# Kernel optimization log

Measured on AMD Instinct MI355X. Metric: run time of the kernel, lower is better.

The kernel has to match this reference:

```python
import jax, jax.numpy as jnp
import numpy as np

NUM_EMBEDDINGS = 1024
EMBEDDING_DIM = 64
COMMITMENT_COST = 0.25


def setup_inputs() -> dict:
    key = jax.random.key(0)
    k1, k2 = jax.random.split(key)
    inputs = jax.random.normal(k1, (16, 64, 64, 64), dtype=jnp.float32)
    codebook = jax.random.normal(k2, (EMBEDDING_DIM, NUM_EMBEDDINGS), dtype=jnp.float32) * 0.01
    return {"inputs": inputs, "codebook": codebook}


def reference(inputs, codebook):
    # flatten exactly as torch: reshape(-1, D) on (B,C,H,W)
    flat = inputs.reshape(-1, EMBEDDING_DIM)  # [N, D]
    distances = (jnp.sum(flat * flat, axis=1, keepdims=True)
                 + jnp.sum(codebook * codebook, axis=0, keepdims=True)
                 - 2.0 * jnp.matmul(flat, codebook))
    encoding_indices = jnp.argmin(distances, axis=1)  # [N]
    quantized = codebook[:, encoding_indices].T.reshape(inputs.shape)
    # losses (MSE over all elements)
    codebook_loss = jnp.mean((jax.lax.stop_gradient(quantized) - inputs) ** 2)
    commitment_loss = COMMITMENT_COST * jnp.mean((quantized - jax.lax.stop_gradient(inputs)) ** 2)
    # perplexity from codebook usage histogram
    n = encoding_indices.shape[0]
    counts = jnp.zeros((NUM_EMBEDDINGS,), dtype=jnp.float32).at[encoding_indices].add(1.0)
    avg_probs = counts / n
    entropy = -jnp.sum(avg_probs * jnp.log(avg_probs + 1e-10))
    perplexity = jnp.exp(entropy)
    # straight-through estimator
    ste = inputs + jax.lax.stop_gradient(quantized - inputs)
    return (ste, perplexity, codebook_loss, commitment_loss,
            encoding_indices.reshape(inputs.shape[0], -1))
```

## Files before the change

kernel.cpp:

```cpp
#include <hip/hip_runtime.h>

typedef __attribute__((ext_vector_type(8))) short short8;
typedef __attribute__((ext_vector_type(4))) float f32x4;

#define N_ROWS   65536
#define DIM      64
#define K_CODES  1024
#define TOTAL_ELEMS 4194304
#define THETA    1e-3f
#define ROWS_PB  64


__device__ __forceinline__ unsigned short f2bf(float f) {
    union { float f; unsigned int u; } c; c.f = f;
    unsigned int u = c.u;
    return (unsigned short)((u + 0x7fffu + ((u >> 16) & 1u)) >> 16);
}
__device__ __forceinline__ float bf2f(unsigned short b) {
    union { unsigned int u; float f; } c; c.u = ((unsigned int)b) << 16;
    return c.f;
}
__device__ __forceinline__ f32x4 MFMA(short8 a, short8 b, f32x4 c) {
    return __builtin_amdgcn_mfma_f32_16x16x32_bf16(a, b, c, 0, 0, 0);
}

__global__ __launch_bounds__(64) void k_prep(const float* __restrict__ cb,
                                             float* __restrict__ norms,
                                             int* __restrict__ counts,
                                             float* __restrict__ cbT,
                                             unsigned short* __restrict__ cb_hi,
                                             unsigned short* __restrict__ cb_lo,
                                             int* __restrict__ flagcnt) {
    int k = blockIdx.x * 64 + threadIdx.x;
    float v[64];
#pragma unroll
    for (int d = 0; d < DIM; ++d) v[d] = cb[d * K_CODES + k];
    float s = __fmul_rn(v[0], v[0]);
#pragma unroll
    for (int d = 1; d < DIM; ++d) s = __fadd_rn(s, __fmul_rn(v[d], v[d]));
    norms[k] = s;
#pragma unroll
    for (int d = 0; d < DIM; ++d) {
        cbT[k * DIM + d] = v[d];
        float t = -2.0f * v[d];
        unsigned short hb = f2bf(t);
        cb_hi[k * DIM + d] = hb;
        cb_lo[k * DIM + d] = f2bf(t - bf2f(hb));
    }
    counts[k] = 0;
    if (k == 0) flagcnt[0] = 0;
}

__global__ __launch_bounds__(256, 2) void k_assign(const float* __restrict__ x,
                                                   const float* __restrict__ norms,
                                                   const unsigned short* __restrict__ cb_hi,
                                                   const unsigned short* __restrict__ cb_lo,
                                                   int* __restrict__ idx_out,
                                                   int* __restrict__ flagcnt,
                                                   int* __restrict__ flaglist) {
    __shared__ __align__(16) unsigned short xs_hi[64 * 64];
    __shared__ __align__(16) unsigned short xs_lo[64 * 64];
    __shared__ float xxs[64];
    __shared__ float mv1[4][64];
    __shared__ float mv2[4][64];
    __shared__ int   mk1[4][64];

    const int tid = threadIdx.x;
    const int r0 = blockIdx.x * 64;
    const int wave = tid >> 6, lane = tid & 63;
    const int lr = lane & 15, lg = lane >> 4;

#pragma unroll
    for (int i = 0; i < 2; ++i) {
        int c = i * 256 + tid;
        int row = c >> 3, ch = c & 7;
        const float4* src = reinterpret_cast<const float4*>(x + (size_t)(r0 + row) * DIM + ch * 8);
        float4 f0 = src[0], f1 = src[1];
        float f[8] = {f0.x, f0.y, f0.z, f0.w, f1.x, f1.y, f1.z, f1.w};
        union { short8 v; unsigned short u[8]; } h, l;
#pragma unroll
        for (int j = 0; j < 8; ++j) {
            unsigned short hb = f2bf(f[j]);
            h.u[j] = hb;
            l.u[j] = f2bf(f[j] - bf2f(hb));
        }
        int eo = row * 64 + ((((ch * 16) ^ ((row & 7) << 4))) >> 1);
        *reinterpret_cast<short8*>(&xs_hi[eo]) = h.v;
        *reinterpret_cast<short8*>(&xs_lo[eo]) = l.v;
    }
    if (lane < 16) {
        int row = wave * 16 + lane;
        const float* xr = x + (size_t)(r0 + row) * DIM;
        float r[8];
#pragma unroll
        for (int j = 0; j < 8; ++j) { float v = xr[j]; r[j] = __fmul_rn(v, v); }
#pragma unroll
        for (int m = 1; m < 8; ++m)
#pragma unroll
            for (int j = 0; j < 8; ++j) { float v = xr[8 * m + j]; r[j] = __fadd_rn(r[j], __fmul_rn(v, v)); }
        float t01 = __fadd_rn(r[0], r[1]), t23 = __fadd_rn(r[2], r[3]);
        float t45 = __fadd_rn(r[4], r[5]), t67 = __fadd_rn(r[6], r[7]);
        xxs[row] = __fadd_rn(__fadd_rn(t01, t23), __fadd_rn(t45, t67));
    }
    __syncthreads();

    short8 a_hi[4][2], a_lo[4][2];
#pragma unroll
    for (int rt = 0; rt < 4; ++rt)
#pragma unroll
        for (int kh = 0; kh < 2; ++kh) {
            int row = rt * 16 + lr;
            int bo = (kh * 64 + lg * 16) ^ ((row & 7) << 4);
            int eo = row * 64 + (bo >> 1);
            a_hi[rt][kh] = *reinterpret_cast<const short8*>(&xs_hi[eo]);
            a_lo[rt][kh] = *reinterpret_cast<const short8*>(&xs_lo[eo]);
        }
    float xxv[16];
#pragma unroll
    for (int rt = 0; rt < 4; ++rt)
#pragma unroll
        for (int r = 0; r < 4; ++r) xxv[rt * 4 + r] = xxs[rt * 16 + lg * 4 + r];

    float v1[16], v2[16]; int k1[16];
#pragma unroll
    for (int i = 0; i < 16; ++i) { v1[i] = 3.4e38f; v2[i] = 3.4e38f; k1[i] = 0; }

    const short8* ph = reinterpret_cast<const short8*>(cb_hi) + (size_t)(wave * 256 + lr) * 8;
    const short8* pl = reinterpret_cast<const short8*>(cb_lo) + (size_t)(wave * 256 + lr) * 8;
    const float*  pe = norms + wave * 256 + lr;

    short8 nh0 = ph[lg], nh1 = ph[4 + lg];
    short8 nl0 = pl[lg], nl1 = pl[4 + lg];
    float  nee = *pe;

    for (int ct = 0; ct < 16; ++ct) {
        short8 h0 = nh0, h1 = nh1, l0 = nl0, l1 = nl1;
        float ee = nee;
        if (ct < 15) {
            ph += 128; pl += 128; pe += 16;
            nh0 = ph[lg]; nh1 = ph[4 + lg];
            nl0 = pl[lg]; nl1 = pl[4 + lg];
            nee = *pe;
        }
        int code = wave * 256 + ct * 16 + lr;

#pragma unroll
        for (int rt = 0; rt < 4; ++rt) {
            f32x4 acc;
            acc[0] = __fadd_rn(xxv[rt * 4 + 0], ee);
            acc[1] = __fadd_rn(xxv[rt * 4 + 1], ee);
            acc[2] = __fadd_rn(xxv[rt * 4 + 2], ee);
            acc[3] = __fadd_rn(xxv[rt * 4 + 3], ee);
            __builtin_amdgcn_s_setprio(1);
            acc = MFMA(a_hi[rt][0], h0, acc);
            acc = MFMA(a_hi[rt][1], h1, acc);
            acc = MFMA(a_hi[rt][0], l0, acc);
            acc = MFMA(a_hi[rt][1], l1, acc);
            acc = MFMA(a_lo[rt][0], h0, acc);
            acc = MFMA(a_lo[rt][1], h1, acc);
            __builtin_amdgcn_s_setprio(0);
#pragma unroll
            for (int r = 0; r < 4; ++r) {
                int i = rt * 4 + r;
                float d = acc[r];
                v2[i] = __builtin_amdgcn_fmed3f(d, v1[i], v2[i]);
                bool lt = d < v1[i];
                k1[i] = lt ? code : k1[i];
                v1[i] = fminf(v1[i], d);
            }
        }
    }

#pragma unroll
    for (int i = 0; i < 16; ++i) {
        float a1 = v1[i], a2 = v2[i]; int ak = k1[i];
#pragma unroll
        for (int off = 1; off <= 8; off <<= 1) {
            float o1 = __shfl_xor(a1, off);
            float o2 = __shfl_xor(a2, off);
            int   ok = __shfl_xor(ak, off);
            float n2 = fminf(fmaxf(a1, o1), fminf(a2, o2));
            if (o1 < a1 || (o1 == a1 && ok < ak)) { a1 = o1; ak = ok; }
            a2 = n2;
        }
        if (lr == 0) {
            int row = (i >> 2) * 16 + lg * 4 + (i & 3);
            mv1[wave][row] = a1; mv2[wave][row] = a2; mk1[wave][row] = ak;
        }
    }
    __syncthreads();

    if (tid < 64) {
        float V1 = mv1[0][tid], V2 = mv2[0][tid]; int K1 = mk1[0][tid];
#pragma unroll
        for (int w = 1; w < 4; ++w) {
            float a1 = mv1[w][tid], a2 = mv2[w][tid]; int ak = mk1[w][tid];
            float n2 = fminf(fmaxf(V1, a1), fminf(V2, a2));
            if (a1 < V1) { V1 = a1; K1 = ak; }
            V2 = n2;
        }
        int rg = r0 + tid;
        idx_out[rg] = K1;
        if (V2 - V1 <= THETA) {
            int p = atomicAdd(flagcnt, 1);
            flaglist[p] = rg;
        }
    }
}

__global__ __launch_bounds__(256) void k_exact(const float* __restrict__ x,
                                               const float* __restrict__ cb,
                                               const float* __restrict__ norms,
                                               const int* __restrict__ flagcnt,
                                               const int* __restrict__ flaglist,
                                               int* __restrict__ idx) {
    __shared__ __align__(16) float xrow[8][64];
    __shared__ float xxs[8];
    __shared__ int rlist[8];
    __shared__ float lv[8][4];
    __shared__ int   lk[8][4];

    const int tid = threadIdx.x;
    const int lane = tid & 63, wv = tid >> 6;
    const int cnt = flagcnt[0];
    const int ngroups = (cnt + 7) >> 3;

    for (int g = blockIdx.x; g < ngroups; g += gridDim.x) {
        const int base = g * 8;
        const int rem = min(8, cnt - base);
        __syncthreads();
        if (tid < 8)
            rlist[tid] = flaglist[base + ((tid < rem) ? tid : 0)];
        __syncthreads();
#pragma unroll
        for (int i = 0; i < 2; ++i) {
            int e = i * 256 + tid;
            int r = e >> 6, d = e & 63;
            xrow[r][d] = x[(size_t)rlist[r] * DIM + d];
        }
        __syncthreads();
        if (tid < 8) {
            float rr[8];
#pragma unroll
            for (int j = 0; j < 8; ++j) { float v = xrow[tid][j]; rr[j] = __fmul_rn(v, v); }
#pragma unroll
            for (int m = 1; m < 8; ++m)
#pragma unroll
                for (int j = 0; j < 8; ++j) { float v = xrow[tid][8 * m + j]; rr[j] = __fadd_rn(rr[j], __fmul_rn(v, v)); }
            float t01 = __fadd_rn(rr[0], rr[1]), t23 = __fadd_rn(rr[2], rr[3]);
            float t45 = __fadd_rn(rr[4], rr[5]), t67 = __fadd_rn(rr[6], rr[7]);
            xxs[tid] = __fadd_rn(__fadd_rn(t01, t23), __fadd_rn(t45, t67));
        }
        __syncthreads();

        double acc[8][4];
#pragma unroll
        for (int r = 0; r < 8; ++r)
#pragma unroll
            for (int j = 0; j < 4; ++j) acc[r][j] = 0.0;

        for (int dc = 0; dc < DIM; dc += 4) {
            float4 xv[8];
#pragma unroll
            for (int r = 0; r < 8; ++r)
                xv[r] = *reinterpret_cast<const float4*>(&xrow[r][dc]);
            float c[4][4];
#pragma unroll
            for (int dd = 0; dd < 4; ++dd)
#pragma unroll
                for (int j = 0; j < 4; ++j)
                    c[j][dd] = cb[(size_t)(dc + dd) * K_CODES + j * 256 + tid];
#pragma unroll
            for (int j = 0; j < 4; ++j)
#pragma unroll
                for (int r = 0; r < 8; ++r) {
                    acc[r][j] += (double)xv[r].x * (double)c[j][0];
                    acc[r][j] += (double)xv[r].y * (double)c[j][1];
                    acc[r][j] += (double)xv[r].z * (double)c[j][2];
                    acc[r][j] += (double)xv[r].w * (double)c[j][3];
                }
        }

#pragma unroll
        for (int r = 0; r < 8; ++r) {
            float xx = xxs[r];
            float bv = 3.4e38f; int bk = 0x7fffffff;
#pragma unroll
            for (int j = 0; j < 4; ++j) {
                int k = j * 256 + tid;
                float m = (float)acc[r][j];
                float dist = __fsub_rn(__fadd_rn(xx, norms[k]), __fmul_rn(2.0f, m));
                if (dist < bv) { bv = dist; bk = k; }
            }
#pragma unroll
            for (int off = 1; off <= 32; off <<= 1) {
                float ov = __shfl_xor(bv, off); int ok = __shfl_xor(bk, off);
                if (ov < bv || (ov == bv && ok < bk)) { bv = ov; bk = ok; }
            }
            if (lane == 0) { lv[r][wv] = bv; lk[r][wv] = bk; }
        }
        __syncthreads();
        if (tid < rem) {
            float bv = lv[tid][0]; int bk = lk[tid][0];
#pragma unroll
            for (int w = 1; w < 4; ++w)
                if (lv[tid][w] < bv || (lv[tid][w] == bv && lk[tid][w] < bk)) { bv = lv[tid][w]; bk = lk[tid][w]; }
            idx[rlist[tid]] = bk;
        }
    }
}

__global__ __launch_bounds__(256) void k_quant(const float* __restrict__ x,
                                               const float* __restrict__ cbT,
                                               const int* __restrict__ idx,
                                               float* __restrict__ ste,
                                               float* __restrict__ partials,
                                               int* __restrict__ counts,
                                               float* __restrict__ idxf) {
    int t  = blockIdx.x * 256 + threadIdx.x;
    int e  = t << 2;
    int n  = e >> 6;
    int dc = e & 63;
    float4 xv = *reinterpret_cast<const float4*>(x + e);
    int k = idx[n];
    float4 qv = *reinterpret_cast<const float4*>(cbT + (size_t)k * DIM + dc);

    float4 sv;
    sv.x = xv.x + (qv.x - xv.x);
    sv.y = xv.y + (qv.y - xv.y);
    sv.z = xv.z + (qv.z - xv.z);
    sv.w = xv.w + (qv.w - xv.w);
    *reinterpret_cast<float4*>(ste + e) = sv;

    if (dc == 0) {
        atomicAdd(&counts[k], 1);
        idxf[n] = (float)k;
    }

    float dx = qv.x - xv.x, dy = qv.y - xv.y, dz = qv.z - xv.z, dw = qv.w - xv.w;
    float s = dx * dx + dy * dy + dz * dz + dw * dw;

#pragma unroll
    for (int off = 32; off >= 1; off >>= 1) s += __shfl_down(s, off);
    __shared__ float red[4];
    int wave = threadIdx.x >> 6, lane = threadIdx.x & 63;
    if (lane == 0) red[wave] = s;
    __syncthreads();
    if (threadIdx.x == 0)
        partials[blockIdx.x] = (red[0] + red[1]) + (red[2] + red[3]);
}

__global__ __launch_bounds__(1024) void k_final(const float* __restrict__ partials,
                                                const int* __restrict__ counts,
                                                float* __restrict__ out_scalars) {
    int tid = threadIdx.x;
    float s = 0.f;
    for (int i = tid; i < 4096; i += 1024) s += partials[i];
#pragma unroll
    for (int off = 32; off >= 1; off >>= 1) s += __shfl_down(s, off);
    __shared__ float wsum[16];
    int wave = tid >> 6, lane = tid & 63;
    if (lane == 0) wsum[wave] = s;

    float c = (float)counts[tid];
    float p = c * (1.0f / 65536.0f);
    float t = -p * logf(p + 1e-10f);
#pragma unroll
    for (int off = 32; off >= 1; off >>= 1) t += __shfl_down(t, off);
    __shared__ float esum[16];
    if (lane == 0) esum[wave] = t;
    __syncthreads();

    if (tid == 0) {
        float total = 0.f, ent = 0.f;
        for (int w = 0; w < 16; ++w) { total += wsum[w]; ent += esum[w]; }
        float mean = total * (1.0f / (float)TOTAL_ELEMS);
        out_scalars[0] = expf(ent);
        out_scalars[1] = mean;
        out_scalars[2] = 0.25f * mean;
    }
}

extern "C" void kernel_launch(void* const* d_in, const int* in_sizes, int n_in,
                              void* d_out, int out_size, void* d_ws, size_t ws_size,
                              hipStream_t stream) {
    const float* x  = (const float*)d_in[0];
    const float* cb = (const float*)d_in[1];
    float* out = (float*)d_out;
    float* ws  = (float*)d_ws;

    float* norms    = ws;
    int*   idx      = (int*)(ws + 1024);
    int*   counts   = (int*)(ws + 66560);
    float* partials = ws + 67584;
    float* cbT      = ws + 71680;
    unsigned short* cb_hi = (unsigned short*)(ws + 137216);
    unsigned short* cb_lo = (unsigned short*)(ws + 169984);
    int*   flagcnt  = (int*)(ws + 202752);
    int*   flaglist = (int*)(ws + 202753);

    float* ste     = out;
    float* scalars = out + TOTAL_ELEMS;
    float* idxf    = out + TOTAL_ELEMS + 3;

    k_prep  <<<16,    64, 0, stream>>>(cb, norms, counts, cbT, cb_hi, cb_lo, flagcnt);
    k_assign<<<1024, 256, 0, stream>>>(x, norms, cb_hi, cb_lo, idx, flagcnt, flaglist);
    k_exact <<<1024, 256, 0, stream>>>(x, cb, norms, flagcnt, flaglist, idx);
    k_quant <<<4096, 256, 0, stream>>>(x, cbT, idx, ste, partials, counts, idxf);
    k_final <<<1,   1024, 0, stream>>>(partials, counts, scalars);
}
```

Baseline: 112.3 us.

## Stage codebook tiles into LDS via async global_load_lds double buffering

Measured after the change: 108.2 us. 1.04x faster.

```diff
diff --git a/kernel.cpp b/kernel.cpp
--- a/kernel.cpp
+++ b/kernel.cpp
@@ -22,6 +22,18 @@
 }
 __device__ __forceinline__ f32x4 MFMA(short8 a, short8 b, f32x4 c) {
     return __builtin_amdgcn_mfma_f32_16x16x32_bf16(a, b, c, 0, 0, 0);
+}
+
+__device__ __forceinline__ void stage_b(const unsigned short* __restrict__ cb,
+                                        unsigned short* lds, int code16base, int lane) {
+    const unsigned int* s = reinterpret_cast<const unsigned int*>(cb + (size_t)code16base * 64);
+    unsigned int* l = reinterpret_cast<unsigned int*>(lds);
+    int p0 = lane;
+    int g0 = (p0 & ~7) | ((p0 ^ (p0 >> 3)) & 7);
+    __builtin_amdgcn_global_load_lds(s + g0 * 4, l, 16, 0, 0);
+    int p1 = 64 + lane;
+    int g1 = (p1 & ~7) | ((p1 ^ (p1 >> 3)) & 7);
+    __builtin_amdgcn_global_load_lds(s + g1 * 4, l + 256, 16, 0, 0);
 }
 
 __global__ __launch_bounds__(64) void k_prep(const float* __restrict__ cb,
@@ -60,6 +72,9 @@
                                                    int* __restrict__ flaglist) {
     __shared__ __align__(16) unsigned short xs_hi[64 * 64];
     __shared__ __align__(16) unsigned short xs_lo[64 * 64];
+    __shared__ __align__(16) unsigned short bsh_hi[8 * 1024];
+    __shared__ __align__(16) unsigned short bsh_lo[8 * 1024];
+    __shared__ float nshf[1024];
     __shared__ float xxs[64];
     __shared__ float mv1[4][64];
     __shared__ float mv2[4][64];
@@ -102,7 +117,22 @@
         float t45 = __fadd_rn(r[4], r[5]), t67 = __fadd_rn(r[6], r[7]);
         xxs[row] = __fadd_rn(__fadd_rn(t01, t23), __fadd_rn(t45, t67));
     }
+#pragma unroll
+    for (int i = 0; i < 4; ++i) {
+        int o = (wave << 8) + (i << 6) + lane;
+        nshf[o] = norms[o];
+    }
     __syncthreads();
+
+    const int cbase = wave * 256;
+    unsigned short* bh0 = bsh_hi + (wave * 2) * 1024;
+    unsigned short* bh1 = bh0 + 1024;
+    unsigned short* bl0 = bsh_lo + (wave * 2) * 1024;
+    unsigned short* bl1 = bl0 + 1024;
+    stage_b(cb_hi, bh0, cbase,      lane);
+    stage_b(cb_lo, bl0, cbase,      lane);
+    stage_b(cb_hi, bh1, cbase + 16, lane);
+    stage_b(cb_lo, bl1, cbase + 16, lane);
 
     short8 a_hi[4][2], a_lo[4][2];
 #pragma unroll
@@ -125,25 +155,16 @@
 #pragma unroll
     for (int i = 0; i < 16; ++i) { v1[i] = 3.4e38f; v2[i] = 3.4e38f; k1[i] = 0; }
 
-    const short8* ph = reinterpret_cast<const short8*>(cb_hi) + (size_t)(wave * 256 + lr) * 8;
-    const short8* pl = reinterpret_cast<const short8*>(cb_lo) + (size_t)(wave * 256 + lr) * 8;
-    const float*  pe = norms + wave * 256 + lr;
-
-    short8 nh0 = ph[lg], nh1 = ph[4 + lg];
-    short8 nl0 = pl[lg], nl1 = pl[4 + lg];
-    float  nee = *pe;
-
-    for (int ct = 0; ct < 16; ++ct) {
-        short8 h0 = nh0, h1 = nh1, l0 = nl0, l1 = nl1;
-        float ee = nee;
-        if (ct < 15) {
-            ph += 128; pl += 128; pe += 16;
-            nh0 = ph[lg]; nh1 = ph[4 + lg];
-            nl0 = pl[lg]; nl1 = pl[4 + lg];
-            nee = *pe;
-        }
-        int code = wave * 256 + ct * 16 + lr;
-
+    const int pc0 = (((lr << 3) + ((lg)     ^ (lr & 7))) << 3);
+    const int pc1 = (((lr << 3) + ((4 + lg) ^ (lr & 7))) << 3);
+
+    auto consume = [&](int ct_, const unsigned short* bh, const unsigned short* bl) {
+        float ee = nshf[(wave << 8) + (ct_ << 4) + lr];
+        short8 h0 = *reinterpret_cast<const short8*>(bh + pc0);
+        short8 h1 = *reinterpret_cast<const short8*>(bh + pc1);
+        short8 l0 = *reinterpret_cast<const short8*>(bl + pc0);
+        short8 l1 = *reinterpret_cast<const short8*>(bl + pc1);
+        int code = cbase + (ct_ << 4) + lr;
 #pragma unroll
         for (int rt = 0; rt < 4; ++rt) {
             f32x4 acc;
@@ -169,7 +190,22 @@
                 v1[i] = fminf(v1[i], d);
             }
         }
-    }
+    };
+
+    for (int ct = 0; ct < 14; ++ct) {
+        asm volatile("s_waitcnt vmcnt(4)" ::: "memory");
+        unsigned short* bh = (ct & 1) ? bh1 : bh0;
+        unsigned short* bl = (ct & 1) ? bl1 : bl0;
+        consume(ct, bh, bl);
+        asm volatile("s_waitcnt lgkmcnt(0)" ::: "memory");
+        __builtin_amdgcn_sched_barrier(0);
+        stage_b(cb_hi, bh, cbase + (ct + 2) * 16, lane);
+        stage_b(cb_lo, bl, cbase + (ct + 2) * 16, lane);
+    }
+    asm volatile("s_waitcnt vmcnt(4)" ::: "memory");
+    consume(14, bh0, bl0);
+    asm volatile("s_waitcnt vmcnt(0)" ::: "memory");
+    consume(15, bh1, bl1);
 
 #pragma unroll
     for (int i = 0; i < 16; ++i) {
```
